# Kernel tuning notes

Hardware: AMD Instinct MI355X
Metric: run time of the kernel (lower is better)

## Reference

```python
import jax, jax.numpy as jnp
import numpy as np

B, S, D, H = 2, 2048, 2048, 16
HD = D // H  # 128


def apply_rotary(xq, xk, cos, sin):
    # xq, xk: [B, S, H, HD]; cos, sin: [S, HD//2]
    def rot(x):
        xr = x.astype(jnp.float32).reshape(*x.shape[:-1], -1, 2)  # [B,S,H,HD/2,2]
        xe, xo = xr[..., 0], xr[..., 1]
        c = cos[None, :, None, :]
        s = sin[None, :, None, :]
        out_e = xe * c - xo * s
        out_o = xe * s + xo * c
        out = jnp.stack([out_e, out_o], axis=-1).reshape(x.shape)
        return out.astype(x.dtype)
    return rot(xq), rot(xk)


def setup_inputs() -> dict:
    key = jax.random.key(0)
    ks = jax.random.split(key, 8)
    x = jax.random.normal(ks[0], (B, S, D), dtype=jnp.float32)
    scale = 1.0 / np.sqrt(D)
    wq = jax.random.normal(ks[1], (D, D), dtype=jnp.float32) * scale
    wk = jax.random.normal(ks[2], (D, D), dtype=jnp.float32) * scale
    wv = jax.random.normal(ks[3], (D, D), dtype=jnp.float32) * scale
    wo = jax.random.normal(ks[4], (D, D), dtype=jnp.float32) * scale
    # RoPE frequencies (standard LLaMA): theta = 10000
    inv_freq = 1.0 / (10000.0 ** (np.arange(0, HD, 2, dtype=np.float32) / HD))
    t = np.arange(S, dtype=np.float32)
    ang = np.outer(t, inv_freq)  # [S, HD/2]
    freqs_cos = jnp.asarray(np.cos(ang))
    freqs_sin = jnp.asarray(np.sin(ang))
    # causal additive mask [1,1,S,S]
    neg = jnp.full((S, S), -1e9, dtype=jnp.float32)
    mask = jnp.triu(neg, k=1)[None, None, :, :]
    return {"x": x, "start_pos": 0, "freqs_cos": freqs_cos, "freqs_sin": freqs_sin,
            "mask": mask, "wq": wq, "wk": wk, "wv": wv, "wo": wo}


def reference(x, start_pos, freqs_cos, freqs_sin, mask, wq, wk, wv, wo):
    bsz, seqlen, dim = x.shape
    xq = (x @ wq.T).reshape(bsz, seqlen, H, HD)
    xk = (x @ wk.T).reshape(bsz, seqlen, H, HD)
    xv = (x @ wv.T).reshape(bsz, seqlen, H, HD)
    xq, xk = apply_rotary(xq, xk, freqs_cos, freqs_sin)
    # [B,H,S,HD]
    q = xq.transpose(0, 2, 1, 3)
    k = xk.transpose(0, 2, 1, 3)
    v = xv.transpose(0, 2, 1, 3)
    scores = jnp.einsum('bhqd,bhkd->bhqk', q, k) / jnp.sqrt(jnp.float32(HD))
    scores = scores + mask
    probs = jax.nn.softmax(scores.astype(jnp.float32), axis=-1).astype(q.dtype)
    out = jnp.einsum('bhqk,bhkd->bhqd', probs, v)
    out = out.transpose(0, 2, 1, 3).reshape(bsz, seqlen, dim)
    return out @ wo.T
```

## Files before the change

### kernel.cpp

```cpp
#include <hip/hip_runtime.h>
#include <cstdint>

typedef unsigned short u16;
typedef __attribute__((ext_vector_type(8))) short bf16x8;
typedef __attribute__((ext_vector_type(4))) float f32x4;

#define S_LEN 2048
#define DM    2048
#define NH    16
#define HDIM  128

__device__ __forceinline__ u16 f2bf(float f) {
  union { float f; unsigned u; } v; v.f = f;
  unsigned r = v.u + 0x7fffu + ((v.u >> 16) & 1u);
  return (u16)(r >> 16);
}
__device__ __forceinline__ float bf2f(u16 h) {
  union { unsigned u; float f; } v; v.u = ((unsigned)h) << 16;
  return v.f;
}

typedef __attribute__((address_space(3))) void lds_void_t;
typedef const __attribute__((address_space(1))) void gbl_void_t;
__device__ __forceinline__ void gload_lds16(const void* g, void* l) {
  __builtin_amdgcn_global_load_lds((gbl_void_t*)g, (lds_void_t*)l, 16, 0, 0);
}

#define VMCNTN(nn) asm volatile("s_waitcnt vmcnt(%0)" :: "n"(nn) : "memory")
#define LGKMCNT0() asm volatile("s_waitcnt lgkmcnt(0)" ::: "memory")

__global__ void cvt5_k(const float* s0, u16* d0, int n0,
                       const float* s1, u16* d1, int n1,
                       const float* s2, u16* d2, int n2,
                       const float* s3, u16* d3, int n3,
                       const float* s4, u16* d4, int n4) {
  const int stride = gridDim.x * blockDim.x;
  const int tid = blockIdx.x * blockDim.x + threadIdx.x;
#define CVT(S, D, N)                                        \
  for (int i = tid; i < ((N) >> 2); i += stride) {          \
    float4 v = ((const float4*)(S))[i];                     \
    ushort4 o;                                              \
    o.x = f2bf(v.x); o.y = f2bf(v.y);                       \
    o.z = f2bf(v.z); o.w = f2bf(v.w);                       \
    ((ushort4*)(D))[i] = o;                                 \
  }
  CVT(s0, d0, n0) CVT(s1, d1, n1) CVT(s2, d2, n2)
  CVT(s3, d3, n3) CVT(s4, d4, n4)
#undef CVT
}

template <int BM, int BN, int M, int N, int K, typename CT, int MODE>
__global__ __launch_bounds__(512, 2) void gemm8(const u16* __restrict__ A,
                                                const u16* __restrict__ Bm,
                                                CT* __restrict__ C,
                                                const float* __restrict__ fc,
                                                const float* __restrict__ fs,
                                                u16* __restrict__ qtp,
                                                u16* __restrict__ ktp) {
  constexpr int PWM = BM / 2, PWN = BN / 4;
  constexpr int MR = PWM / 16, NR = PWN / 16;
  constexpr int LA = BM / 128, LB = BN / 128;
  constexpr int VMK = LA + LB;
  constexpr int LDSA = BM * 32, LDSB = BN * 32;
  constexpr int nbn = N / BN, nbm = M / BM;
  constexpr int nwg = nbm * nbn;
  constexpr int GM = 8;
  __shared__ u16 sA[2 * LDSA];
  __shared__ u16 sB[2 * LDSB];

  const int t = threadIdx.x;
  const int lane = t & 63, wid = t >> 6;
  const int r0 = lane & 15, kq = lane >> 4;
  const int wr = wid >> 2, wc = wid & 3;

  const int bid = blockIdx.x;
  const int wgl = (bid & 7) * (nwg >> 3) + (bid >> 3);
  const int gid = wgl / (GM * nbn);
  const int rem = wgl % (GM * nbn);
  const long tile_m = (long)(gid * GM + (rem & (GM - 1))) * BM;
  const long tile_n = (long)(rem >> 3) * BN;

  constexpr int NPH = K / 32;

  const int swzcol = ((t & 3) ^ ((t >> 3) & 3)) * 8;
  const u16* gA = A + (tile_m + (t >> 2)) * (long)K + swzcol;
  const u16* gB = Bm + (tile_n + (t >> 2)) * (long)K + swzcol;

  auto stage = [&](int h) {
    u16* ba = &sA[(h & 1) * LDSA] + wid * 512;
    u16* bb = &sB[(h & 1) * LDSB] + wid * 512;
    const long coff = (long)h * 32;
#pragma unroll
    for (int r = 0; r < LA; ++r)
      gload_lds16(gA + (long)(r * 128) * K + coff, ba + r * 4096);
#pragma unroll
    for (int r = 0; r < LB; ++r)
      gload_lds16(gB + (long)(r * 128) * K + coff, bb + r * 4096);
  };

  const int rdslot = (kq ^ ((r0 >> 1) & 3)) * 8;
  const int aoff = (wr * PWM + r0) * 32 + rdslot;
  const int boff = (wc * PWN + r0) * 32 + rdslot;

  f32x4 acc[MR][NR];
#pragma unroll
  for (int m = 0; m < MR; ++m)
#pragma unroll
    for (int n = 0; n < NR; ++n) acc[m][n] = (f32x4){0.f, 0.f, 0.f, 0.f};

  stage(0); stage(1);
  VMCNTN(VMK);
  __builtin_amdgcn_s_barrier();

  for (int h = 0; h < NPH; ++h) {
    const u16* ra = &sA[(h & 1) * LDSA] + aoff;
    const u16* rb = &sB[(h & 1) * LDSB] + boff;
    bf16x8 a[MR], b[NR];
#pragma unroll
    for (int m = 0; m < MR; ++m) a[m] = *(const bf16x8*)(ra + m * 512);
#pragma unroll
    for (int n = 0; n < NR; ++n) b[n] = *(const bf16x8*)(rb + n * 512);
    LGKMCNT0();
    __builtin_amdgcn_s_barrier();
    stage(h + 2);
    __builtin_amdgcn_s_setprio(1);
#pragma unroll
    for (int m = 0; m < MR; ++m)
#pragma unroll
      for (int n = 0; n < NR; ++n)
        acc[m][n] = __builtin_amdgcn_mfma_f32_16x16x32_bf16(a[m], b[n],
                                                            acc[m][n], 0, 0, 0);
    __builtin_amdgcn_s_setprio(0);
    VMCNTN(VMK);
    __builtin_amdgcn_s_barrier();
  }

  if constexpr (MODE == 1) {
    const int z = (int)(tile_n >> 11);
    if (z == 2) {
#pragma unroll
      for (int m = 0; m < MR; ++m)
#pragma unroll
        for (int n = 0; n < NR; ++n)
#pragma unroll
          for (int r = 0; r < 4; ++r) {
            long grow = tile_m + wr * PWM + m * 16 + kq * 4 + r;
            long gcol = tile_n + wc * PWN + n * 16 + r0;
            C[grow * N + gcol] = (CT)f2bf(acc[m][n][r]);
          }
    } else {
      const float qsc = 0.12751743202f;
#pragma unroll
      for (int m = 0; m < MR; ++m)
#pragma unroll
        for (int n = 0; n < NR; ++n)
#pragma unroll
          for (int r = 0; r < 4; ++r) {
            long grow = tile_m + wr * PWM + m * 16 + kq * 4 + r;
            long gcol = tile_n + wc * PWN + n * 16 + r0;
            int srow = (int)(grow & 2047), bidx = (int)(grow >> 11);
            int h = ((int)gcol >> 7) & 15, hd = (int)gcol & 127;
            float v = acc[m][n][r];
            float partner = __shfl_xor(v, 1);
            int hd2 = hd >> 1;
            float c = fc[srow * 64 + hd2], sn = fs[srow * 64 + hd2];
            float res = (r0 & 1) ? (partner * sn + v * c)
                                 : (v * c - partner * sn);
            if (z == 0) res *= qsc;
            u16* dst = z ? ktp : qtp;
            dst[((long)(bidx * 16 + h) * S_LEN + srow) * HDIM + hd] = f2bf(res);
          }
    }
  } else {
#pragma unroll
    for (int m = 0; m < MR; ++m)
#pragma unroll
      for (int n = 0; n < NR; ++n)
#pragma unroll
        for (int r = 0; r < 4; ++r) {
          long grow = tile_m + wr * PWM + m * 16 + kq * 4 + r;
          long gcol = tile_n + wc * PWN + n * 16 + r0;
          float v = acc[m][n][r];
          if constexpr (sizeof(CT) == 2) C[grow * N + gcol] = (CT)f2bf(v);
          else                           C[grow * N + gcol] = v;
        }
  }
}

__global__ void vtrans_k(const u16* __restrict__ qkv, u16* __restrict__ vt) {
  __shared__ u16 tile[64][65];
  int bh = blockIdx.z;
  int b = bh >> 4, h = bh & 15;
  int s0 = blockIdx.x * 64, d0 = blockIdx.y * 64;
  int tx = threadIdx.x, ty = threadIdx.y;
#pragma unroll
  for (int i = 0; i < 64; i += 4) {
    int s = s0 + ty + i;
    tile[ty + i][tx] = qkv[((long)(b * S_LEN + s)) * 6144 + 4096 + h * HDIM + d0 + tx];
  }
  __syncthreads();
#pragma unroll
  for (int i = 0; i < 64; i += 4) {
    int d = d0 + ty + i;
    vt[((long)bh * HDIM + d) * S_LEN + s0 + tx] = tile[tx][ty + i];
  }
}

__global__ __launch_bounds__(64) void flash_k(const u16* __restrict__ qt,
                                              const u16* __restrict__ kt,
                                              const u16* __restrict__ vt,
                                              u16* __restrict__ attn) {
  constexpr int PS = 40;
  __shared__ u16 pbuf[2][32 * PS];
  const int lane = threadIdx.x & 63;
  const int r0 = lane & 15, kq = lane >> 4;
  const int bh = blockIdx.x, b = bh >> 4, h = bh & 15;
  const int seg = (gridDim.y - 1) - blockIdx.y;
  const int q0w = seg * 32;
  const int crow = kq * 4;

  const u16* qb = qt + ((long)bh * S_LEN + q0w) * HDIM;
  const u16* kb = kt + (long)bh * S_LEN * HDIM;
  const u16* vb = vt + (long)bh * HDIM * S_LEN;
  u16* pb0 = &pbuf[0][0];
  u16* pb1 = &pbuf[1][0];

  bf16x8 aq[2][4];
#pragma unroll
  for (int qc = 0; qc < 2; ++qc)
#pragma unroll
    for (int kk = 0; kk < 4; ++kk)
      aq[qc][kk] = *(const bf16x8*)(qb + (qc * 16 + r0) * HDIM + kk * 32 + kq * 8);

  f32x4 o[2][8];
  float mrow[2] = {-1e30f, -1e30f}, lrow[2] = {0.f, 0.f};
#pragma unroll
  for (int qc = 0; qc < 2; ++qc)
#pragma unroll
    for (int dt = 0; dt < 8; ++dt) o[qc][dt] = (f32x4){0.f, 0.f, 0.f, 0.f};

  bf16x8 bkA[2][4], bkB[2][4], bvA[8], bvB[8];
  f32x4 saccA[2][2], saccB[2][2];

  auto loadK = [&](bf16x8 (&dst)[2][4], int kv) {
#pragma unroll
    for (int kc = 0; kc < 2; ++kc)
#pragma unroll
      for (int kk = 0; kk < 4; ++kk)
        dst[kc][kk] = *(const bf16x8*)(kb + (long)(kv + kc * 16 + r0) * HDIM + kk * 32 + kq * 8);
  };
  auto loadV = [&](bf16x8 (&dst)[8], int kv) {
#pragma unroll
    for (int dt = 0; dt < 8; ++dt)
      dst[dt] = *(const bf16x8*)(vb + (long)(dt * 16 + r0) * S_LEN + kv + kq * 8);
  };
  auto qk = [&](bf16x8 (&kf)[2][4], f32x4 (&sacc)[2][2]) {
    __builtin_amdgcn_s_setprio(1);
#pragma unroll
    for (int kc = 0; kc < 2; ++kc) {
      f32x4 a0 = (f32x4){0.f, 0.f, 0.f, 0.f};
      f32x4 a1 = (f32x4){0.f, 0.f, 0.f, 0.f};
#pragma unroll
      for (int kk = 0; kk < 4; ++kk) {
        a0 = __builtin_amdgcn_mfma_f32_16x16x32_bf16(kf[kc][kk], aq[0][kk], a0, 0, 0, 0);
        a1 = __builtin_amdgcn_mfma_f32_16x16x32_bf16(kf[kc][kk], aq[1][kk], a1, 0, 0, 0);
      }
      sacc[kc][0] = a0; sacc[kc][1] = a1;
    }
    __builtin_amdgcn_s_setprio(0);
  };
  auto softmax_store = [&](f32x4 (&sacc)[2][2], int kv0, u16* pb) {
    const bool diag = (kv0 == q0w);
#pragma unroll
    for (int qc = 0; qc < 2; ++qc) {
      float s[2][4];
#pragma unroll
      for (int kc = 0; kc < 2; ++kc)
#pragma unroll
        for (int r = 0; r < 4; ++r) {
          float v = sacc[kc][qc][r];
          if (diag && (kc * 16 + crow + r > qc * 16 + r0)) v = -1e30f;
          s[kc][r] = v;
        }
      float pm = fmaxf(fmaxf(fmaxf(s[0][0], s[0][1]), fmaxf(s[0][2], s[0][3])),
                       fmaxf(fmaxf(s[1][0], s[1][1]), fmaxf(s[1][2], s[1][3])));
      pm = fmaxf(pm, __shfl_xor(pm, 16));
      pm = fmaxf(pm, __shfl_xor(pm, 32));
      if (!__all(pm - mrow[qc] <= 11.5416f)) {
        float mnew = fmaxf(mrow[qc], pm);
        float co = exp2f(mrow[qc] - mnew);
        mrow[qc] = mnew;
        lrow[qc] *= co;
        float cod[4];
#pragma unroll
        for (int r = 0; r < 4; ++r)
          cod[r] = __shfl(co, (lane & 48) | (crow + r));
#pragma unroll
        for (int dt = 0; dt < 8; ++dt)
#pragma unroll
          for (int r = 0; r < 4; ++r)
            o[qc][dt][r] *= cod[r];
      }
      float p[2][4];
      float rs = 0.f;
#pragma unroll
      for (int kc = 0; kc < 2; ++kc)
#pragma unroll
        for (int r = 0; r < 4; ++r) {
          p[kc][r] = exp2f(s[kc][r] - mrow[qc]);
          rs += p[kc][r];
        }
      rs += __shfl_xor(rs, 16);
      rs += __shfl_xor(rs, 32);
      lrow[qc] += rs;
#pragma unroll
      for (int kc = 0; kc < 2; ++kc) {
        unsigned w0, w1;
        asm("v_cvt_pk_bf16_f32 %0, %1, %2" : "=v"(w0) : "v"(p[kc][0]), "v"(p[kc][1]));
        asm("v_cvt_pk_bf16_f32 %0, %1, %2" : "=v"(w1) : "v"(p[kc][2]), "v"(p[kc][3]));
        uint2 w; w.x = w0; w.y = w1;
        *(uint2*)(pb + (qc * 16 + r0) * PS + kc * 16 + crow) = w;
      }
    }
  };
  auto pv = [&](const u16* pb, bf16x8 (&bv)[8]) {
    bf16x8 pa0 = *(const bf16x8*)(pb + r0 * PS + kq * 8);
    bf16x8 pa1 = *(const bf16x8*)(pb + (16 + r0) * PS + kq * 8);
    __builtin_amdgcn_s_setprio(1);
#pragma unroll
    for (int dt = 0; dt < 8; ++dt) {
      o[0][dt] = __builtin_amdgcn_mfma_f32_16x16x32_bf16(pa0, bv[dt], o[0][dt], 0, 0, 0);
      o[1][dt] = __builtin_amdgcn_mfma_f32_16x16x32_bf16(pa1, bv[dt], o[1][dt], 0, 0, 0);
    }
    __builtin_amdgcn_s_setprio(0);
  };

  loadK(bkA, 0);
  if (32 <= q0w) loadK(bkB, 32);
  qk(bkA, saccA);
  int kv0 = 0;
  for (;;) {
    {
      const bool more = (kv0 + 32 <= q0w);
      loadV(bvA, kv0);
      softmax_store(saccA, kv0, pb0);
      if (more) qk(bkB, saccB);
      if (kv0 + 64 <= q0w) loadK(bkA, kv0 + 64);
      pv(pb0, bvA);
      kv0 += 32;
      if (!more) break;
    }
    {
      const bool more = (kv0 + 32 <= q0w);
      loadV(bvB, kv0);
      softmax_store(saccB, kv0, pb1);
      if (more) qk(bkA, saccA);
      if (kv0 + 64 <= q0w) loadK(bkB, kv0 + 64);
      pv(pb1, bvB);
      kv0 += 32;
      if (!more) break;
    }
  }

#pragma unroll
  for (int qc = 0; qc < 2; ++qc) {
    float linv[4];
#pragma unroll
    for (int r = 0; r < 4; ++r)
      linv[r] = 1.0f / __shfl(lrow[qc], (lane & 48) | (crow + r));
#pragma unroll
    for (int dt = 0; dt < 8; ++dt)
#pragma unroll
      for (int r = 0; r < 4; ++r) {
        int srow = q0w + qc * 16 + crow + r;
        attn[((long)(b * S_LEN + srow)) * DM + h * HDIM + dt * 16 + r0] =
            f2bf(o[qc][dt][r] * linv[r]);
      }
  }
}

extern "C" void kernel_launch(void* const* d_in, const int* in_sizes, int n_in,
                              void* d_out, int out_size, void* d_ws, size_t ws_size,
                              hipStream_t stream) {
  (void)in_sizes; (void)n_in; (void)out_size; (void)ws_size;
  const float* x  = (const float*)d_in[0];
  const float* fc = (const float*)d_in[2];
  const float* fs = (const float*)d_in[3];
  const float* wq = (const float*)d_in[5];
  const float* wk = (const float*)d_in[6];
  const float* wv = (const float*)d_in[7];
  const float* wo = (const float*)d_in[8];
  float* out = (float*)d_out;

  u16* xb   = (u16*)d_ws;
  u16* wqkv = xb + 8388608;
  u16* wob  = wqkv + 12582912;
  u16* qkv  = wob + 4194304;
  u16* qt   = qkv + 25165824;
  u16* kt   = qt + 8388608;
  u16* vt   = kt + 8388608;
  u16* attn = qkv;

  cvt5_k<<<2048, 256, 0, stream>>>(x, xb, 8388608,
                                   wq, wqkv, 4194304,
                                   wk, wqkv + 4194304, 4194304,
                                   wv, wqkv + 8388608, 4194304,
                                   wo, wob, 4194304);

  gemm8<128, 256, 4096, 6144, 2048, u16, 1><<<768, 512, 0, stream>>>(
      xb, wqkv, qkv, fc, fs, qt, kt);

  vtrans_k<<<dim3(32, 2, 32), dim3(64, 4), 0, stream>>>(qkv, vt);

  flash_k<<<dim3(32, 64), 64, 0, stream>>>(qt, kt, vt, attn);

  gemm8<128, 256, 4096, 2048, 2048, float, 0><<<256, 512, 0, stream>>>(
      attn, wob, out, nullptr, nullptr, nullptr, nullptr);
}
```

Baseline: 317.7 us.

## Split flash attention KV range into two chunks with combine kernel

Each query segment's KV loop is split into two halves processed by separate workgroups (grid z=2). Each half writes its unnormalized output plus row max and sum, and a new combine kernel merges them into the final attention tensor. The aim is to shorten the long causal tail workgroups and raise parallelism, since the flash kernel used only 64-thread workgroups over 2048 blocks. The cost is an extra kernel launch plus the global traffic for the partial outputs. The partials are stored in bf16 before merging, which may slightly reduce precision.

```diff
diff --git a/kernel.cpp b/kernel.cpp
--- a/kernel.cpp
+++ b/kernel.cpp
@@ -209,15 +209,24 @@
 __global__ __launch_bounds__(64) void flash_k(const u16* __restrict__ qt,
                                               const u16* __restrict__ kt,
                                               const u16* __restrict__ vt,
-                                              u16* __restrict__ attn) {
+                                              u16* __restrict__ op0,
+                                              u16* __restrict__ op1,
+                                              float* __restrict__ ml) {
   constexpr int PS = 40;
   __shared__ u16 pbuf[2][32 * PS];
   const int lane = threadIdx.x & 63;
   const int r0 = lane & 15, kq = lane >> 4;
-  const int bh = blockIdx.x, b = bh >> 4, h = bh & 15;
+  const int bh = blockIdx.x;
   const int seg = (gridDim.y - 1) - blockIdx.y;
+  const int chunk = blockIdx.z;
   const int q0w = seg * 32;
   const int crow = kq * 4;
+
+  const int nst = seg + 1;
+  const int beg = chunk ? (nst >> 1) : 0;
+  const int endst = chunk ? nst : (nst >> 1);
+  const int kbeg = beg * 32;
+  const int lastkv = (endst - 1) * 32;
 
   const u16* qb = qt + ((long)bh * S_LEN + q0w) * HDIM;
   const u16* kb = kt + (long)bh * S_LEN * HDIM;
@@ -335,48 +344,82 @@
     __builtin_amdgcn_s_setprio(0);
   };
 
-  loadK(bkA, 0);
-  if (32 <= q0w) loadK(bkB, 32);
-  qk(bkA, saccA);
-  int kv0 = 0;
-  for (;;) {
-    {
-      const bool more = (kv0 + 32 <= q0w);
-      loadV(bvA, kv0);
-      softmax_store(saccA, kv0, pb0);
-      if (more) qk(bkB, saccB);
-      if (kv0 + 64 <= q0w) loadK(bkA, kv0 + 64);
-      pv(pb0, bvA);
-      kv0 += 32;
-      if (!more) break;
-    }
-    {
-      const bool more = (kv0 + 32 <= q0w);
-      loadV(bvB, kv0);
-      softmax_store(saccB, kv0, pb1);
-      if (more) qk(bkA, saccA);
-      if (kv0 + 64 <= q0w) loadK(bkB, kv0 + 64);
-      pv(pb1, bvB);
-      kv0 += 32;
-      if (!more) break;
-    }
-  }
-
-#pragma unroll
-  for (int qc = 0; qc < 2; ++qc) {
-    float linv[4];
-#pragma unroll
-    for (int r = 0; r < 4; ++r)
-      linv[r] = 1.0f / __shfl(lrow[qc], (lane & 48) | (crow + r));
+  if (endst > beg) {
+    loadK(bkA, kbeg);
+    if (kbeg + 32 <= lastkv) loadK(bkB, kbeg + 32);
+    qk(bkA, saccA);
+    int kv0 = kbeg;
+    for (;;) {
+      {
+        const bool more = (kv0 + 32 <= lastkv);
+        loadV(bvA, kv0);
+        softmax_store(saccA, kv0, pb0);
+        if (more) qk(bkB, saccB);
+        if (kv0 + 64 <= lastkv) loadK(bkA, kv0 + 64);
+        pv(pb0, bvA);
+        kv0 += 32;
+        if (!more) break;
+      }
+      {
+        const bool more = (kv0 + 32 <= lastkv);
+        loadV(bvB, kv0);
+        softmax_store(saccB, kv0, pb1);
+        if (more) qk(bkA, saccA);
+        if (kv0 + 64 <= lastkv) loadK(bkB, kv0 + 64);
+        pv(pb1, bvB);
+        kv0 += 32;
+        if (!more) break;
+      }
+    }
+  }
+
+  u16* op = chunk ? op1 : op0;
+#pragma unroll
+  for (int qc = 0; qc < 2; ++qc)
 #pragma unroll
     for (int dt = 0; dt < 8; ++dt)
 #pragma unroll
       for (int r = 0; r < 4; ++r) {
         int srow = q0w + qc * 16 + crow + r;
-        attn[((long)(b * S_LEN + srow)) * DM + h * HDIM + dt * 16 + r0] =
-            f2bf(o[qc][dt][r] * linv[r]);
-      }
-  }
+        op[((long)bh * S_LEN + srow) * HDIM + dt * 16 + r0] = f2bf(o[qc][dt][r]);
+      }
+  if (kq == 0) {
+    float* mlp = ml + (long)chunk * (32 * S_LEN * 2);
+#pragma unroll
+    for (int qc = 0; qc < 2; ++qc) {
+      long row = (long)bh * S_LEN + q0w + qc * 16 + r0;
+      mlp[row * 2]     = mrow[qc];
+      mlp[row * 2 + 1] = lrow[qc];
+    }
+  }
+}
+
+__global__ __launch_bounds__(256) void comb_k(const u16* __restrict__ op0,
+                                              const u16* __restrict__ op1,
+                                              const float* __restrict__ ml,
+                                              u16* __restrict__ attn) {
+  const long g = (long)blockIdx.x * 256 + threadIdx.x;
+  const long row = g >> 4;
+  const int c0 = (int)(g & 15) * 8;
+  const int bh = (int)(row >> 11), s = (int)(row & 2047);
+  const int b = bh >> 4, h = bh & 15;
+
+  const float m0 = ml[row * 2], l0 = ml[row * 2 + 1];
+  const float m1 = ml[32 * S_LEN * 2 + row * 2], l1 = ml[32 * S_LEN * 2 + row * 2 + 1];
+  const float m = fmaxf(m0, m1);
+  const float w0 = exp2f(m0 - m), w1 = exp2f(m1 - m);
+  const float inv = 1.0f / (l0 * w0 + l1 * w1);
+
+  bf16x8 a = *(const bf16x8*)(op0 + row * HDIM + c0);
+  bf16x8 c = *(const bf16x8*)(op1 + row * HDIM + c0);
+  ushort4 out[2];
+#pragma unroll
+  for (int j = 0; j < 8; ++j) {
+    float v = (bf2f((u16)a[j]) * w0 + bf2f((u16)c[j]) * w1) * inv;
+    ((u16*)out)[j] = f2bf(v);
+  }
+  *(ushort4*)(attn + ((long)(b * S_LEN + s)) * DM + h * HDIM + c0) = out[0];
+  *(ushort4*)(attn + ((long)(b * S_LEN + s)) * DM + h * HDIM + c0 + 4) = out[1];
 }
 
 extern "C" void kernel_launch(void* const* d_in, const int* in_sizes, int n_in,
@@ -400,6 +443,9 @@
   u16* kt   = qt + 8388608;
   u16* vt   = kt + 8388608;
   u16* attn = qkv;
+  u16*   op0 = xb;
+  u16*   op1 = wqkv;
+  float* ml  = (float*)(wqkv + 8388608);
 
   cvt5_k<<<2048, 256, 0, stream>>>(x, xb, 8388608,
                                    wq, wqkv, 4194304,
@@ -412,7 +458,9 @@
 
   vtrans_k<<<dim3(32, 2, 32), dim3(64, 4), 0, stream>>>(qkv, vt);
 
-  flash_k<<<dim3(32, 64), 64, 0, stream>>>(qt, kt, vt, attn);
+  flash_k<<<dim3(32, 64, 2), 64, 0, stream>>>(qt, kt, vt, op0, op1, ml);
+
+  comb_k<<<4096, 256, 0, stream>>>(op0, op1, ml, attn);
 
   gemm8<128, 256, 4096, 2048, 2048, float, 0><<<256, 512, 0, stream>>>(
       attn, wob, out, nullptr, nullptr, nullptr, nullptr);
```

New measurement: 331.1 us. 1.04x slower.
